# Kernel optimization log

Hardware: AMD Instinct MI355X
Metric: run time of the kernel (lower is better)

The kernel has to match this reference:

```python
import jax, jax.numpy as jnp
import numpy as np

BINS = 10


def setup_inputs() -> dict:
    key = jax.random.key(0)
    k1, k2 = jax.random.split(key)
    x = jax.random.uniform(k1, (16384, 2048), dtype=jnp.float32, minval=1e-4, maxval=1.0 - 1e-4)
    target = jax.random.uniform(k2, (16384, 2048), dtype=jnp.float32)
    return {"x": x, "target": target}


def reference(x, target):
    # gradient magnitude (detached in original)
    g = jnp.abs(jax.lax.stop_gradient(x) - target)
    # _g2bin: floor(g * (bins - 0.0001)) -> integer bin ids in [0, BINS-1]
    bin_idx = jnp.floor(g * (BINS - 1e-4)).astype(jnp.int32)
    # histogram (replaces the serialized per-bin python loop)
    bin_count = jnp.bincount(bin_idx.ravel(), length=BINS).astype(jnp.float32)
    N = x.shape[0] * x.shape[1]
    nonempty_bins = jnp.sum(bin_count > 0).astype(jnp.float32)
    gd = jnp.clip(bin_count * nonempty_bins, 1.0, None)
    beta = N / gd  # [BINS]
    # BCE on probabilities, reweighted by gathered beta
    loss = -(target * jnp.log(x) + (1.0 - target) * jnp.log(1.0 - x))
    loss = loss * beta[bin_idx]
    return jnp.mean(loss)
```

## Files before the change

### kernel.cpp

```cpp
#include <hip/hip_runtime.h>

#define BINS 10
#define NTHR 9

__device__ __forceinline__ void accum_elem(float xx, float tt, float sc_mul,
                                           float* __restrict__ S,
                                           unsigned* __restrict__ C,
                                           float& s_total) {
    float y = fabsf(xx - tt) * sc_mul;
    float om = 1.0f - xx;
    float l1 = __log2f(xx);
    float l2 = __log2f(om);
    float s = __builtin_fmaf(tt, l1 - l2, l2);
    s_total += s;
#pragma unroll
    for (int j = 0; j < NTHR; ++j) {
        bool p = (y >= (float)(j + 1));
        S[j] += p ? s : 0.0f;
        C[j] += p ? 1u : 0u;
    }
}

__global__ __launch_bounds__(256) void ghm_partial(
    const float* __restrict__ x, const float* __restrict__ t,
    float* __restrict__ psum, unsigned* __restrict__ pcnt,
    int n4, long long n_total, int nblocks)
{
    float S[NTHR];
    unsigned C[NTHR];
    float s_total = 0.0f;
#pragma unroll
    for (int j = 0; j < NTHR; ++j) { S[j] = 0.0f; C[j] = 0u; }

    const float sc_mul = 9.9999f;
    const float4* __restrict__ x4 = (const float4*)x;
    const float4* __restrict__ t4 = (const float4*)t;
    int tid = blockIdx.x * blockDim.x + threadIdx.x;
    int stride = gridDim.x * blockDim.x;

    int i = tid;
    if (i < n4) {
        float4 cx = x4[i];
        float4 ct = t4[i];
        for (;;) {
            int nx = i + stride;
            bool more = nx < n4;
            float4 px, pt;
            if (more) { px = x4[nx]; pt = t4[nx]; }
            accum_elem(cx.x, ct.x, sc_mul, S, C, s_total);
            accum_elem(cx.y, ct.y, sc_mul, S, C, s_total);
            accum_elem(cx.z, ct.z, sc_mul, S, C, s_total);
            accum_elem(cx.w, ct.w, sc_mul, S, C, s_total);
            if (!more) break;
            cx = px; ct = pt; i = nx;
        }
    }
    long long tail_base = (long long)n4 * 4;
    long long rem = n_total - tail_base;
    if ((long long)tid < rem) {
        accum_elem(x[tail_base + tid], t[tail_base + tid], sc_mul, S, C, s_total);
    }

#pragma unroll
    for (int off = 32; off > 0; off >>= 1) s_total += __shfl_down(s_total, off, 64);
#pragma unroll
    for (int j = 0; j < NTHR; ++j) {
#pragma unroll
        for (int off = 32; off > 0; off >>= 1) {
            S[j] += __shfl_down(S[j], off, 64);
            C[j] += (unsigned)__shfl_down((int)C[j], off, 64);
        }
    }

    __shared__ float s_sum[4][NTHR + 1];
    __shared__ unsigned s_cnt[4][NTHR];
    int lane = threadIdx.x & 63;
    int wv = threadIdx.x >> 6;
    if (lane == 0) {
        s_sum[wv][0] = s_total;
#pragma unroll
        for (int j = 0; j < NTHR; ++j) { s_sum[wv][j + 1] = S[j]; s_cnt[wv][j] = C[j]; }
    }
    __syncthreads();
    if (threadIdx.x < NTHR + 1) {
        int r = threadIdx.x;
        float s = 0.0f;
#pragma unroll
        for (int w = 0; w < 4; ++w) s += s_sum[w][r];
        psum[(size_t)r * nblocks + blockIdx.x] = s;
        if (r < NTHR) {
            unsigned c = 0u;
#pragma unroll
            for (int w = 0; w < 4; ++w) c += s_cnt[w][r];
            pcnt[(size_t)r * nblocks + blockIdx.x] = c;
        }
    }
}

__global__ __launch_bounds__(256) void ghm_final(
    const float* __restrict__ psum, const unsigned* __restrict__ pcnt,
    float* __restrict__ out, int nblocks, float Nf, long long N)
{
    float rs[NTHR + 1];
    unsigned rc[NTHR];
#pragma unroll
    for (int r = 0; r < NTHR + 1; ++r) rs[r] = 0.0f;
#pragma unroll
    for (int r = 0; r < NTHR; ++r) rc[r] = 0u;

    for (int i = threadIdx.x; i < nblocks; i += 256) {
#pragma unroll
        for (int r = 0; r < NTHR + 1; ++r) rs[r] += psum[(size_t)r * nblocks + i];
#pragma unroll
        for (int r = 0; r < NTHR; ++r) rc[r] += pcnt[(size_t)r * nblocks + i];
    }

#pragma unroll
    for (int r = 0; r < NTHR + 1; ++r) {
#pragma unroll
        for (int off = 32; off > 0; off >>= 1) rs[r] += __shfl_down(rs[r], off, 64);
    }
#pragma unroll
    for (int r = 0; r < NTHR; ++r) {
#pragma unroll
        for (int off = 32; off > 0; off >>= 1) rc[r] += (unsigned)__shfl_down((int)rc[r], off, 64);
    }

    __shared__ float s_sum[4][NTHR + 1];
    __shared__ unsigned s_cnt[4][NTHR];
    int lane = threadIdx.x & 63;
    int wv = threadIdx.x >> 6;
    if (lane == 0) {
#pragma unroll
        for (int r = 0; r < NTHR + 1; ++r) s_sum[wv][r] = rs[r];
#pragma unroll
        for (int r = 0; r < NTHR; ++r) s_cnt[wv][r] = rc[r];
    }
    __syncthreads();

    if (threadIdx.x == 0) {
        float Sc[BINS + 1];
        float Cc[BINS + 1];
#pragma unroll
        for (int r = 0; r < NTHR + 1; ++r) {
            float s = 0.0f;
#pragma unroll
            for (int w = 0; w < 4; ++w) s += s_sum[w][r];
            Sc[r] = s;
        }
        Sc[BINS] = 0.0f;
        Cc[0] = (float)N;
#pragma unroll
        for (int r = 0; r < NTHR; ++r) {
            unsigned c = 0u;
#pragma unroll
            for (int w = 0; w < 4; ++w) c += s_cnt[w][r];
            Cc[r + 1] = (float)c;
        }
        Cc[BINS] = 0.0f;

        float cnt[BINS], sb[BINS];
        float nonempty = 0.0f;
#pragma unroll
        for (int b = 0; b < BINS; ++b) {
            cnt[b] = Cc[b] - Cc[b + 1];
            sb[b] = Sc[b] - Sc[b + 1];
            nonempty += (cnt[b] > 0.0f) ? 1.0f : 0.0f;
        }
        float total = 0.0f;
#pragma unroll
        for (int b = 0; b < BINS; ++b) {
            float gd = cnt[b] * nonempty;
            gd = gd < 1.0f ? 1.0f : gd;
            total += sb[b] * (Nf / gd);
        }
        const float LN2 = 0.69314718055994530942f;
        out[0] = -LN2 * total / Nf;
    }
}

extern "C" void kernel_launch(void* const* d_in, const int* in_sizes, int n_in,
                              void* d_out, int out_size, void* d_ws, size_t ws_size,
                              hipStream_t stream) {
    const float* x = (const float*)d_in[0];
    const float* t = (const float*)d_in[1];
    float* out = (float*)d_out;

    long long N = (long long)in_sizes[0];
    int n4 = (int)(N / 4);

    int nblocks = 2048;
    size_t per_block = (size_t)(NTHR + 1) * sizeof(float) + (size_t)NTHR * sizeof(unsigned);
    size_t maxb = ws_size / per_block;
    if ((size_t)nblocks > maxb) nblocks = (int)maxb;
    if (nblocks < 1) nblocks = 1;

    float* psum = (float*)d_ws;
    unsigned* pcnt = (unsigned*)(psum + (size_t)(NTHR + 1) * nblocks);

    ghm_partial<<<nblocks, 256, 0, stream>>>(x, t, psum, pcnt, n4, N, nblocks);
    ghm_final<<<1, 256, 0, stream>>>(psum, pcnt, out, nblocks, (float)N, N);
}
```

Before: 286.9 us.

## Count bins with wave ballot-popcount and unroll loads two float4s per iteration

Per-thread bin counters are replaced by wave-level counts built from ballot and popcount, so each wave holds its counts in uniform registers and the count shuffle reduction is dropped. The main loop now handles two float4 pairs per iteration with software prefetch, followed by a guarded remainder pass and a guarded scalar tail pass on block 0. Launch bounds now request 4 blocks per CU. The goal is fewer vector ALU ops and registers per element and more memory parallelism, at the cost of extra ballot and scalar instructions per threshold.

```diff
diff --git a/kernel.cpp b/kernel.cpp
--- a/kernel.cpp
+++ b/kernel.cpp
@@ -3,62 +3,95 @@
 #define BINS 10
 #define NTHR 9
 
-__device__ __forceinline__ void accum_elem(float xx, float tt, float sc_mul,
+template<bool GUARD>
+__device__ __forceinline__ void accum_elem(float xx, float tt, bool live,
                                            float* __restrict__ S,
-                                           unsigned* __restrict__ C,
-                                           float& s_total) {
-    float y = fabsf(xx - tt) * sc_mul;
-    float om = 1.0f - xx;
+                                           unsigned* __restrict__ wcnt,
+                                           float& s_total)
+{
+    float y = fabsf(xx - tt) * 9.9999f;
     float l1 = __log2f(xx);
-    float l2 = __log2f(om);
+    float l2 = __log2f(1.0f - xx);
     float s = __builtin_fmaf(tt, l1 - l2, l2);
+    if (GUARD) {
+        y = live ? y : -1.0f;
+        s = live ? s : 0.0f;
+    }
     s_total += s;
 #pragma unroll
     for (int j = 0; j < NTHR; ++j) {
         bool p = (y >= (float)(j + 1));
         S[j] += p ? s : 0.0f;
-        C[j] += p ? 1u : 0u;
-    }
-}
-
-__global__ __launch_bounds__(256) void ghm_partial(
+        wcnt[j] += (unsigned)__popcll(__ballot(p));
+    }
+}
+
+template<bool GUARD>
+__device__ __forceinline__ void accum4(float4 xv, float4 tv, bool live,
+                                       float* __restrict__ S,
+                                       unsigned* __restrict__ wcnt, float& st)
+{
+    accum_elem<GUARD>(xv.x, tv.x, live, S, wcnt, st);
+    accum_elem<GUARD>(xv.y, tv.y, live, S, wcnt, st);
+    accum_elem<GUARD>(xv.z, tv.z, live, S, wcnt, st);
+    accum_elem<GUARD>(xv.w, tv.w, live, S, wcnt, st);
+}
+
+__global__ __launch_bounds__(256, 4) void ghm_partial(
     const float* __restrict__ x, const float* __restrict__ t,
     float* __restrict__ psum, unsigned* __restrict__ pcnt,
     int n4, long long n_total, int nblocks)
 {
     float S[NTHR];
-    unsigned C[NTHR];
+    unsigned wcnt[NTHR];
     float s_total = 0.0f;
 #pragma unroll
-    for (int j = 0; j < NTHR; ++j) { S[j] = 0.0f; C[j] = 0u; }
-
-    const float sc_mul = 9.9999f;
+    for (int j = 0; j < NTHR; ++j) { S[j] = 0.0f; wcnt[j] = 0u; }
+
     const float4* __restrict__ x4 = (const float4*)x;
     const float4* __restrict__ t4 = (const float4*)t;
-    int tid = blockIdx.x * blockDim.x + threadIdx.x;
-    int stride = gridDim.x * blockDim.x;
-
-    int i = tid;
-    if (i < n4) {
-        float4 cx = x4[i];
-        float4 ct = t4[i];
-        for (;;) {
-            int nx = i + stride;
-            bool more = nx < n4;
-            float4 px, pt;
-            if (more) { px = x4[nx]; pt = t4[nx]; }
-            accum_elem(cx.x, ct.x, sc_mul, S, C, s_total);
-            accum_elem(cx.y, ct.y, sc_mul, S, C, s_total);
-            accum_elem(cx.z, ct.z, sc_mul, S, C, s_total);
-            accum_elem(cx.w, ct.w, sc_mul, S, C, s_total);
+    const int tid = blockIdx.x * blockDim.x + threadIdx.x;
+    const int stride = gridDim.x * blockDim.x;
+    const int iters = n4 / (2 * stride);
+
+    if (iters > 0) {
+        long long i = tid;
+        float4 ax = x4[i],          at_ = t4[i];
+        float4 bx = x4[i + stride], bt  = t4[i + stride];
+        for (int k = 0; ; ++k) {
+            bool more = (k + 1 < iters);
+            long long nx = i + 2LL * stride;
+            float4 cx, ct, dx, dt;
+            if (more) {
+                cx = x4[nx];          ct = t4[nx];
+                dx = x4[nx + stride]; dt = t4[nx + stride];
+            }
+            accum4<false>(ax, at_, true, S, wcnt, s_total);
+            accum4<false>(bx, bt,  true, S, wcnt, s_total);
             if (!more) break;
-            cx = px; ct = pt; i = nx;
-        }
-    }
+            ax = cx; at_ = ct; bx = dx; bt = dt; i = nx;
+        }
+    }
+
+    long long r0 = (long long)tid + (long long)iters * 2LL * stride;
+    long long blk_min = (long long)blockIdx.x * blockDim.x + (long long)iters * 2LL * stride;
+    if (blk_min < n4) {
+#pragma unroll
+        for (int q = 0; q < 2; ++q) {
+            long long r = r0 + (long long)q * stride;
+            bool live = r < n4;
+            int ri = live ? (int)r : 0;
+            float4 xv = x4[ri], tv = t4[ri];
+            accum4<true>(xv, tv, live, S, wcnt, s_total);
+        }
+    }
+
     long long tail_base = (long long)n4 * 4;
-    long long rem = n_total - tail_base;
-    if ((long long)tid < rem) {
-        accum_elem(x[tail_base + tid], t[tail_base + tid], sc_mul, S, C, s_total);
+    if (blockIdx.x == 0 && tail_base < n_total) {
+        long long e = tail_base + threadIdx.x;
+        bool live = e < n_total;
+        long long ei = live ? e : (n_total - 1);
+        accum_elem<true>(x[ei], t[ei], live, S, wcnt, s_total);
     }
 
 #pragma unroll
@@ -66,10 +99,7 @@
 #pragma unroll
     for (int j = 0; j < NTHR; ++j) {
 #pragma unroll
-        for (int off = 32; off > 0; off >>= 1) {
-            S[j] += __shfl_down(S[j], off, 64);
-            C[j] += (unsigned)__shfl_down((int)C[j], off, 64);
-        }
+        for (int off = 32; off > 0; off >>= 1) S[j] += __shfl_down(S[j], off, 64);
     }
 
     __shared__ float s_sum[4][NTHR + 1];
@@ -79,7 +109,7 @@
     if (lane == 0) {
         s_sum[wv][0] = s_total;
 #pragma unroll
-        for (int j = 0; j < NTHR; ++j) { s_sum[wv][j + 1] = S[j]; s_cnt[wv][j] = C[j]; }
+        for (int j = 0; j < NTHR; ++j) { s_sum[wv][j + 1] = S[j]; s_cnt[wv][j] = wcnt[j]; }
     }
     __syncthreads();
     if (threadIdx.x < NTHR + 1) {
@@ -159,8 +189,8 @@
         }
         Cc[BINS] = 0.0f;
 
+        float nonempty = 0.0f;
         float cnt[BINS], sb[BINS];
-        float nonempty = 0.0f;
 #pragma unroll
         for (int b = 0; b < BINS; ++b) {
             cnt[b] = Cc[b] - Cc[b + 1];
```

Result: no change. 289.4 us (+0.9%).
